# Kernel tuning notes

Measured on AMD Instinct MI355X. Metric: run time of the kernel, lower is better.

Reference implementation:

```python
import jax, jax.numpy as jnp
import numpy as np

TEMP = 1.0
EPS = 1e-3  # keras LayerNormalization default epsilon


def _ln(x, g, b):
    m = jnp.mean(x, -1, keepdims=True)
    v = jnp.mean((x - m) ** 2, -1, keepdims=True)
    return g * (x - m) * jax.lax.rsqrt(v + EPS) + b


def setup_inputs() -> dict:
    key = jax.random.key(0)
    ks = jax.random.split(key, 16)
    B, N, C, A, F = 8, 2048, 64, 256, 128
    r = lambda k, s: (jax.random.normal(ks[k], s) * 0.02).astype(jnp.float32)
    z = lambda n: jnp.zeros((n,), jnp.float32)
    return {
        'spatial': jax.random.normal(ks[0], (B, N, C), jnp.float32),
        'frequency': jax.random.normal(ks[1], (B, N, C), jnp.float32),
        'wavelet': jax.random.normal(ks[2], (B, N, C), jnp.float32),
        'Ws': r(3, (C, A)), 'bs': z(A),
        'Wf': r(4, (C, A)), 'bf': z(A),
        'Ww': r(5, (C, A)), 'bw': z(A),
        'g1': jnp.ones((A,), jnp.float32), 'b1': z(A),
        'Wk': r(6, (A, F)), 'bk': z(F),
        'Wq': r(7, (A, F)), 'bq': z(F),
        'Wt': r(8, (A, F)), 'bt': z(F),
        'Wg': r(9, (F + 3, F)), 'bg': z(F),
        'Wfu': r(10, (3 * F, F)), 'bfu': z(F),
        'Wdf': r(11, (F, F)), 'bdf': z(F),
        'g2': jnp.ones((F,), jnp.float32), 'b2': z(F),
    }


def _forward(spatial, frequency, wavelet, Ws, bs, Wf, bf, Ww, bw, g1, b1,
             Wk, bk, Wq, bq, Wt, bt, Wg, bg, Wfu, bfu, Wdf, bdf, g2, b2):
    B = spatial.shape[0]
    # FeatureAlignment: per-domain Dense + shared LayerNorm
    aligned = [
        _ln(spatial @ Ws + bs, g1, b1),
        _ln(frequency @ Wf + bf, g1, b1),
        _ln(wavelet @ Ww + bw, g1, b1),
    ]  # each [B, N, A]
    # DomainCorrelation
    K = [a @ Wk + bk for a in aligned]  # [B, N, F]
    Q = [a @ Wq + bq for a in aligned]
    corr = jnp.zeros((B, 3, 3), spatial.dtype)
    for i in range(3):
        for j in range(i, 3):
            # queries from domain j, keys from domain i (as in original)
            s = jax.nn.softmax(jnp.einsum('bnd,bmd->bnm', Q[j], K[i]) / TEMP, axis=-1)
            m = jnp.mean(s, axis=(1, 2))  # [B]
            corr = corr.at[:, i, j].set(m)
            if i != j:
                corr = corr.at[:, j, i].set(m)
    # NOTE: original applies softmax over the batch axis of the [B] row means
    dw = [jax.nn.softmax(jnp.mean(corr[:, i, :], axis=1)) for i in range(3)]  # each [B]
    # FeatureTransfer
    corr_mean = jnp.mean(corr, axis=1)  # [B, 3]
    enhanced = []
    for a, w in zip(aligned, dw):
        t = a @ Wt + bt  # [B, N, F]
        N = t.shape[1]
        gin = jnp.concatenate([t, jnp.broadcast_to(corr_mean[:, None, :], (B, N, 3))], axis=-1)
        gate = jax.nn.sigmoid(gin @ Wg + bg)
        enhanced.append(t * gate * w[:, None, None])
    fused = jnp.concatenate(enhanced, axis=-1) @ Wfu + bfu  # [B, N, F]
    out = _ln(fused @ Wdf + bdf, g2, b2)
    return out, corr, dw, enhanced


def reference(spatial, frequency, wavelet, Ws, bs, Wf, bf, Ww, bw, g1, b1,
              Wk, bk, Wq, bq, Wt, bt, Wg, bg, Wfu, bfu, Wdf, bdf, g2, b2):
    out, corr, dw, enh = _forward(spatial, frequency, wavelet, Ws, bs, Wf, bf, Ww, bw,
                                  g1, b1, Wk, bk, Wq, bq, Wt, bt, Wg, bg, Wfu, bfu,
                                  Wdf, bdf, g2, b2)
    return (out, corr, dw[0], dw[1], dw[2], enh[0], enh[1], enh[2])
```

## Files before the change

kernel.cpp:

```cpp
#include <hip/hip_runtime.h>
#include <math.h>


typedef __attribute__((ext_vector_type(8))) short short8;
typedef __attribute__((ext_vector_type(4))) float f32x4;
#define MFMA(a, b, c) __builtin_amdgcn_mfma_f32_16x16x32_bf16(a, b, c, 0, 0, 0)

#define NTOK 32
#define XP 72
#define AP 264
#define TP 136
#define PP 12

#define WD0_B 0u
#define WD1_B 32768u
#define WD2_B 65536u
#define WT_B  98304u
#define WG_B  163840u
#define WF0_B 196608u
#define WF1_B 229376u
#define WF2_B 262144u
#define WDF_B 294912u

__device__ __forceinline__ unsigned short bf16rtn(float v) {
    unsigned u = __float_as_uint(v);
    unsigned r = u + 0x7FFFu + ((u >> 16) & 1u);
    return (unsigned short)(r >> 16);
}
__device__ __forceinline__ void split2(float v, unsigned short& h, unsigned short& l) {
    h = bf16rtn(v);
    float hf = __uint_as_float(((unsigned)h) << 16);
    l = bf16rtn(v - hf);
}
__device__ __forceinline__ float bf2f(unsigned short h) {
    return __uint_as_float(((unsigned)h) << 16);
}

__device__ __forceinline__ unsigned cvt_pk_bf16(float a, float b) {
    unsigned r;
    asm("v_cvt_pk_bf16_f32 %0, %1, %2" : "=v"(r) : "v"(a), "v"(b));
    return r;
}
__device__ __forceinline__ void split2pk(float a, float b, unsigned& hp, unsigned& lp) {
    hp = cvt_pk_bf16(a, b);
    const float ha = __uint_as_float(hp << 16);
    const float hb = __uint_as_float(hp & 0xffff0000u);
    lp = cvt_pk_bf16(a - ha, b - hb);
}
__device__ __forceinline__ void stage_x(const f32x4 v,
                                        unsigned short* __restrict__ xh,
                                        unsigned short* __restrict__ xl,
                                        int stok, int sc4) {
    unsigned h01, l01, h23, l23;
    split2pk(v.x, v.y, h01, l01);
    split2pk(v.z, v.w, h23, l23);
    *(uint2*)&xh[stok * XP + sc4] = make_uint2(h01, h23);
    *(uint2*)&xl[stok * XP + sc4] = make_uint2(l01, l23);
}

__global__ __launch_bounds__(256) void prep_kernel(
    const float* __restrict__ Ws, const float* __restrict__ Wf,
    const float* __restrict__ Ww, const float* __restrict__ Wt,
    const float* __restrict__ Wg, const float* __restrict__ Wfu,
    const float* __restrict__ Wdf, unsigned short* __restrict__ ws)
{
    int s = blockIdx.x * 256 + threadIdx.x;
    const float* src; int K, N; unsigned base, S; int fi;
    if (s < 2048)      { src = Ws;            K = 64;  N = 256; base = WD0_B; S = 16384; fi = s; }
    else if (s < 4096) { src = Wf;            K = 64;  N = 256; base = WD1_B; S = 16384; fi = s - 2048; }
    else if (s < 6144) { src = Ww;            K = 64;  N = 256; base = WD2_B; S = 16384; fi = s - 4096; }
    else if (s < 10240){ src = Wt;            K = 256; N = 128; base = WT_B;  S = 32768; fi = s - 6144; }
    else if (s < 12288){ src = Wg;            K = 128; N = 128; base = WG_B;  S = 16384; fi = s - 10240; }
    else if (s < 14336){ src = Wfu;           K = 128; N = 128; base = WF0_B; S = 16384; fi = s - 12288; }
    else if (s < 16384){ src = Wfu + 16384;   K = 128; N = 128; base = WF1_B; S = 16384; fi = s - 14336; }
    else if (s < 18432){ src = Wfu + 32768;   K = 128; N = 128; base = WF2_B; S = 16384; fi = s - 16384; }
    else               { src = Wdf;           K = 128; N = 128; base = WDF_B; S = 16384; fi = s - 18432; }
    const int lane = fi & 63, frag = fi >> 6;
    const int KC = K >> 5;
    const int nt = frag / KC, kc = frag - nt * KC;
    const int n  = nt * 16 + (lane & 15);
    const int k0 = kc * 32 + (lane >> 4) * 8;
    short8 hv, lv;
    #pragma unroll
    for (int j = 0; j < 8; ++j) {
        unsigned short h, l;
        split2(src[(k0 + j) * N + n], h, l);
        hv[j] = (short)h; lv[j] = (short)l;
    }
    *(short8*)&ws[base + (unsigned)fi * 8]     = hv;
    *(short8*)&ws[base + S + (unsigned)fi * 8] = lv;
}

__device__ __forceinline__ void gemm128_d2(
    const unsigned short* __restrict__ wsB, unsigned S,
    const unsigned short* __restrict__ Ph, const unsigned short* __restrict__ Pl,
    int tok0, int tok1, int quad, int wv, int lane, f32x4 acc[2])
{
    short8 Bh[2], Bl[2];
    #pragma unroll
    for (int j = 0; j < 2; ++j) {
        const unsigned short* bp = wsB + ((unsigned)(wv * 4 + j) * 64 + lane) * 8;
        Bh[j] = *(const short8*)bp; Bl[j] = *(const short8*)(bp + S);
    }
    #pragma unroll
    for (int kc = 0; kc < 4; ++kc) {
        const short8 bh = Bh[kc & 1], bl = Bl[kc & 1];
        if (kc + 2 < 4) {
            const unsigned short* bp = wsB + ((unsigned)(wv * 4 + kc + 2) * 64 + lane) * 8;
            Bh[kc & 1] = *(const short8*)bp; Bl[kc & 1] = *(const short8*)(bp + S);
        }
        const int k = kc * 32 + quad * 8;
        const short8 Ah0 = *(const short8*)&Ph[tok0 * TP + k];
        const short8 Al0 = *(const short8*)&Pl[tok0 * TP + k];
        const short8 Ah1 = *(const short8*)&Ph[tok1 * TP + k];
        const short8 Al1 = *(const short8*)&Pl[tok1 * TP + k];
        acc[0] = MFMA(Ah0, bh, acc[0]);
        acc[1] = MFMA(Ah1, bh, acc[1]);
        acc[0] = MFMA(Al0, bh, acc[0]);
        acc[1] = MFMA(Al1, bh, acc[1]);
        acc[0] = MFMA(Ah0, bl, acc[0]);
        acc[1] = MFMA(Ah1, bl, acc[1]);
    }
}

__global__ __launch_bounds__(512) void mega_kernel(
    const float* __restrict__ x0, const float* __restrict__ x1,
    const float* __restrict__ x2,
    const float* __restrict__ bd0, const float* __restrict__ bd1,
    const float* __restrict__ bd2,
    const float* __restrict__ g1, const float* __restrict__ b1,
    const float* __restrict__ bt, const float* __restrict__ Wg,
    const float* __restrict__ bg, const float* __restrict__ bfu,
    const float* __restrict__ bdf, const float* __restrict__ g2,
    const float* __restrict__ b2,
    const unsigned short* __restrict__ ws,
    float* __restrict__ out, float* __restrict__ consts,
    float* __restrict__ e0, float* __restrict__ e1, float* __restrict__ e2)
{
    __shared__ __align__(16) unsigned char smem[54272];
    unsigned short* xh = (unsigned short*)smem;
    unsigned short* xl = xh + 32 * XP;
    unsigned short* th = (unsigned short*)smem;
    unsigned short* tl = th + 32 * TP;
    unsigned short* ah = (unsigned short*)(smem + 17408);
    unsigned short* al = ah + 32 * AP;
    unsigned short* eh = (unsigned short*)(smem + 17408);
    unsigned short* el = eh + 32 * TP;
    float* ostage = (float*)(smem + 17408);
    float* psumS  = (float*)(smem + 51200);
    float* psumQ  = psumS + 32 * PP;

    if (blockIdx.x & 256) __builtin_amdgcn_s_sleep(78);

    const int tid = threadIdx.x, wv = tid >> 6, lane = tid & 63;
    const int lm = lane & 15, quad = lane >> 4;
    const int row0 = blockIdx.x * NTOK;
    const int tok0 = lm, tok1 = lm + 16;
    const int stok = tid >> 4, sc4 = (tid & 15) * 4;

    if (blockIdx.x == 0) {
        if (tid < 72) consts[tid] = 4.8828125e-4f;
        else if (tid < 96) consts[tid] = 0.125f;
    }

    int cA[2]; float g1c[2], b1c[2];
    #pragma unroll
    for (int i = 0; i < 2; ++i) { cA[i] = (wv * 2 + i) * 16 + lm; g1c[i] = g1[cA[i]]; b1c[i] = b1[cA[i]]; }
    const int cT = wv * 16 + lm;
    const float btc = bt[cT];
    const float bgc = bg[cT] + 4.8828125e-4f * (Wg[16384 + cT] + Wg[16512 + cT] + Wg[16640 + cT]);
    const float bdc = bdf[cT], g2c = g2[cT], b2c = b2[cT];
    f32x4 facc[2];
    { const float bv = bfu[cT]; facc[0] = (f32x4){bv, bv, bv, bv}; facc[1] = facc[0]; }

    const float* xs[3]  = {x0, x1, x2};
    const float* bds[3] = {bd0, bd1, bd2};
    float* es[3] = {e0, e1, e2};
    const unsigned WDB[3] = {WD0_B, WD1_B, WD2_B};
    const unsigned WFB[3] = {WF0_B, WF1_B, WF2_B};

    {
        const f32x4 v = __builtin_nontemporal_load(
            (const f32x4*)&xs[0][(row0 + stok) * 64 + sc4]);
        stage_x(v, xh, xl, stok, sc4);
    }
    __syncthreads();

    for (int d = 0; d < 3; ++d) {
        f32x4 acc[2][2];
        {
            const float* bdp = bds[d];
            #pragma unroll
            for (int i = 0; i < 2; ++i) {
                const float bv = bdp[cA[i]];
                acc[i][0] = (f32x4){bv, bv, bv, bv}; acc[i][1] = acc[i][0];
            }
        }
        {
            short8 Bh[2], Bl[2];
            #pragma unroll
            for (int j = 0; j < 2; ++j) {
                const unsigned short* bp = ws + WDB[d] +
                    ((unsigned)((wv * 2 + j) * 2 + 0) * 64 + lane) * 8;
                Bh[j] = *(const short8*)bp; Bl[j] = *(const short8*)(bp + 16384);
            }
            #pragma unroll
            for (int f = 0; f < 4; ++f) {
                const int kc = f >> 1, i = f & 1;
                const short8 bh = Bh[f & 1], bl = Bl[f & 1];
                if (f + 2 < 4) {
                    const int f2 = f + 2;
                    const unsigned short* bp = ws + WDB[d] +
                        ((unsigned)((wv * 2 + (f2 & 1)) * 2 + (f2 >> 1)) * 64 + lane) * 8;
                    Bh[f & 1] = *(const short8*)bp; Bl[f & 1] = *(const short8*)(bp + 16384);
                }
                const int k = kc * 32 + quad * 8;
                const short8 Ah0 = *(const short8*)&xh[tok0 * XP + k];
                const short8 Al0 = *(const short8*)&xl[tok0 * XP + k];
                const short8 Ah1 = *(const short8*)&xh[tok1 * XP + k];
                const short8 Al1 = *(const short8*)&xl[tok1 * XP + k];
                acc[i][0] = MFMA(Ah0, bh, acc[i][0]);
                acc[i][1] = MFMA(Ah1, bh, acc[i][1]);
                acc[i][0] = MFMA(Al0, bh, acc[i][0]);
                acc[i][1] = MFMA(Al1, bh, acc[i][1]);
                acc[i][0] = MFMA(Ah0, bl, acc[i][0]);
                acc[i][1] = MFMA(Ah1, bl, acc[i][1]);
            }
        }
        #pragma unroll
        for (int m = 0; m < 2; ++m)
            #pragma unroll
            for (int r = 0; r < 4; ++r) {
                float s = acc[0][m][r] + acc[1][m][r];
                float q = acc[0][m][r] * acc[0][m][r] + acc[1][m][r] * acc[1][m][r];
                #pragma unroll
                for (int off = 1; off < 16; off <<= 1) {
                    s += __shfl_xor(s, off); q += __shfl_xor(q, off);
                }
                if (lm == 0) {
                    const int row = m * 16 + quad * 4 + r;
                    psumS[row * PP + wv] = s;
                    psumQ[row * PP + wv] = q;
                }
            }
        __syncthreads();

        #pragma unroll
        for (int m = 0; m < 2; ++m)
            #pragma unroll
            for (int r = 0; r < 4; ++r) {
                const int row = m * 16 + quad * 4 + r;
                const float4 s0 = *(const float4*)&psumS[row * PP];
                const float4 s1 = *(const float4*)&psumS[row * PP + 4];
                const float4 q0 = *(const float4*)&psumQ[row * PP];
                const float4 q1 = *(const float4*)&psumQ[row * PP + 4];
                const float S = s0.x + s0.y + s0.z + s0.w + s1.x + s1.y + s1.z + s1.w;
                const float Q = q0.x + q0.y + q0.z + q0.w + q1.x + q1.y + q1.z + q1.w;
                const float mean = S * (1.f / 256.f);
                const float rs = rsqrtf(Q * (1.f / 256.f) - mean * mean + 1e-3f);
                const float v0 = (acc[0][m][r] - mean) * rs * g1c[0] + b1c[0];
                const float v1 = (acc[1][m][r] - mean) * rs * g1c[1] + b1c[1];
                unsigned hp, lp; split2pk(v0, v1, hp, lp);
                ah[row * AP + cA[0]] = (unsigned short)hp;
                ah[row * AP + cA[1]] = (unsigned short)(hp >> 16);
                al[row * AP + cA[0]] = (unsigned short)lp;
                al[row * AP + cA[1]] = (unsigned short)(lp >> 16);
            }
        __syncthreads();

        f32x4 xvn;
        if (d < 2)
            xvn = __builtin_nontemporal_load(
                (const f32x4*)&xs[d + 1][(row0 + stok) * 64 + sc4]);

        f32x4 tac[2];
        tac[0] = (f32x4){btc, btc, btc, btc}; tac[1] = tac[0];
        {
            short8 Bh[2], Bl[2];
            #pragma unroll
            for (int j = 0; j < 2; ++j) {
                const unsigned short* bp = ws + WT_B + ((unsigned)(wv * 8 + j) * 64 + lane) * 8;
                Bh[j] = *(const short8*)bp; Bl[j] = *(const short8*)(bp + 32768);
            }
            #pragma unroll
            for (int kc = 0; kc < 8; ++kc) {
                const short8 bh = Bh[kc & 1], bl = Bl[kc & 1];
                if (kc + 2 < 8) {
                    const unsigned short* bp = ws + WT_B + ((unsigned)(wv * 8 + kc + 2) * 64 + lane) * 8;
                    Bh[kc & 1] = *(const short8*)bp; Bl[kc & 1] = *(const short8*)(bp + 32768);
                }
                const int k = kc * 32 + quad * 8;
                const short8 Ah0 = *(const short8*)&ah[tok0 * AP + k];
                const short8 Al0 = *(const short8*)&al[tok0 * AP + k];
                const short8 Ah1 = *(const short8*)&ah[tok1 * AP + k];
                const short8 Al1 = *(const short8*)&al[tok1 * AP + k];
                tac[0] = MFMA(Ah0, bh, tac[0]);
                tac[1] = MFMA(Ah1, bh, tac[1]);
                tac[0] = MFMA(Al0, bh, tac[0]);
                tac[1] = MFMA(Al1, bh, tac[1]);
                tac[0] = MFMA(Ah0, bl, tac[0]);
                tac[1] = MFMA(Ah1, bl, tac[1]);
            }
        }
        #pragma unroll
        for (int m = 0; m < 2; ++m) {
            const int rb = m * 16 + quad * 4;
            unsigned hp, lp;
            split2pk(tac[m][0], tac[m][1], hp, lp);
            th[rb * TP + cT]       = (unsigned short)hp;
            th[(rb + 1) * TP + cT] = (unsigned short)(hp >> 16);
            tl[rb * TP + cT]       = (unsigned short)lp;
            tl[(rb + 1) * TP + cT] = (unsigned short)(lp >> 16);
            split2pk(tac[m][2], tac[m][3], hp, lp);
            th[(rb + 2) * TP + cT] = (unsigned short)hp;
            th[(rb + 3) * TP + cT] = (unsigned short)(hp >> 16);
            tl[(rb + 2) * TP + cT] = (unsigned short)lp;
            tl[(rb + 3) * TP + cT] = (unsigned short)(lp >> 16);
        }
        __syncthreads();

        f32x4 zac[2];
        zac[0] = (f32x4){bgc, bgc, bgc, bgc}; zac[1] = zac[0];
        gemm128_d2(ws + WG_B, 16384, th, tl, tok0, tok1, quad, wv, lane, zac);

        #pragma unroll
        for (int m = 0; m < 2; ++m) {
            const int rb = m * 16 + quad * 4;
            float e[4];
            #pragma unroll
            for (int r = 0; r < 4; ++r) {
                const int row = rb + r;
                const float tv = bf2f(th[row * TP + cT]) + bf2f(tl[row * TP + cT]);
                e[r] = tv * (1.f / (1.f + __expf(-zac[m][r]))) * 0.125f;
            }
            unsigned hp, lp;
            split2pk(e[0], e[1], hp, lp);
            eh[rb * TP + cT]       = (unsigned short)hp;
            eh[(rb + 1) * TP + cT] = (unsigned short)(hp >> 16);
            el[rb * TP + cT]       = (unsigned short)lp;
            el[(rb + 1) * TP + cT] = (unsigned short)(lp >> 16);
            split2pk(e[2], e[3], hp, lp);
            eh[(rb + 2) * TP + cT] = (unsigned short)hp;
            eh[(rb + 3) * TP + cT] = (unsigned short)(hp >> 16);
            el[(rb + 2) * TP + cT] = (unsigned short)lp;
            el[(rb + 3) * TP + cT] = (unsigned short)(lp >> 16);
        }
        __syncthreads();

        gemm128_d2(ws + WFB[d], 16384, eh, el, tok0, tok1, quad, wv, lane, facc);

        #pragma unroll
        for (int p = 0; p < 2; ++p) {
            const int row = (tid >> 5) + p * 16;
            const int c4 = (tid & 31) * 4;
            const ushort4 h0 = *(const ushort4*)&eh[row * TP + c4];
            const ushort4 l0 = *(const ushort4*)&el[row * TP + c4];
            f32x4 o = {bf2f(h0.x) + bf2f(l0.x), bf2f(h0.y) + bf2f(l0.y),
                       bf2f(h0.z) + bf2f(l0.z), bf2f(h0.w) + bf2f(l0.w)};
            __builtin_nontemporal_store(o, (f32x4*)(es[d] + (row0 + row) * 128 + c4));
        }

        if (d < 2) {
            stage_x(xvn, xh, xl, stok, sc4);
        } else {
            #pragma unroll
            for (int m = 0; m < 2; ++m) {
                const int rb = m * 16 + quad * 4;
                unsigned hp, lp;
                split2pk(facc[m][0], facc[m][1], hp, lp);
                th[rb * TP + cT]       = (unsigned short)hp;
                th[(rb + 1) * TP + cT] = (unsigned short)(hp >> 16);
                tl[rb * TP + cT]       = (unsigned short)lp;
                tl[(rb + 1) * TP + cT] = (unsigned short)(lp >> 16);
                split2pk(facc[m][2], facc[m][3], hp, lp);
                th[(rb + 2) * TP + cT] = (unsigned short)hp;
                th[(rb + 3) * TP + cT] = (unsigned short)(hp >> 16);
                tl[(rb + 2) * TP + cT] = (unsigned short)lp;
                tl[(rb + 3) * TP + cT] = (unsigned short)(lp >> 16);
            }
        }
        __syncthreads();
    }

    f32x4 dac[2];
    dac[0] = (f32x4){bdc, bdc, bdc, bdc}; dac[1] = dac[0];
    gemm128_d2(ws + WDF_B, 16384, th, tl, tok0, tok1, quad, wv, lane, dac);

    #pragma unroll
    for (int m = 0; m < 2; ++m)
        #pragma unroll
        for (int r = 0; r < 4; ++r) {
            float s = dac[m][r];
            float q = dac[m][r] * dac[m][r];
            #pragma unroll
            for (int off = 1; off < 16; off <<= 1) {
                s += __shfl_xor(s, off); q += __shfl_xor(q, off);
            }
            if (lm == 0) {
                const int row = m * 16 + quad * 4 + r;
                psumS[row * PP + wv] = s;
                psumQ[row * PP + wv] = q;
            }
        }
    __syncthreads();
    #pragma unroll
    for (int m = 0; m < 2; ++m)
        #pragma unroll
        for (int r = 0; r < 4; ++r) {
            const int row = m * 16 + quad * 4 + r;
            const float4 s0 = *(const float4*)&psumS[row * PP];
            const float4 s1 = *(const float4*)&psumS[row * PP + 4];
            const float4 q0 = *(const float4*)&psumQ[row * PP];
            const float4 q1 = *(const float4*)&psumQ[row * PP + 4];
            const float S = s0.x + s0.y + s0.z + s0.w + s1.x + s1.y + s1.z + s1.w;
            const float Q = q0.x + q0.y + q0.z + q0.w + q1.x + q1.y + q1.z + q1.w;
            const float mean = S * (1.f / 128.f);
            const float rs = rsqrtf(Q * (1.f / 128.f) - mean * mean + 1e-3f);
            ostage[row * 128 + cT] = (dac[m][r] - mean) * rs * g2c + b2c;
        }
    __syncthreads();
    #pragma unroll
    for (int p = 0; p < 2; ++p) {
        const int row = (tid >> 5) + p * 16;
        const int c4 = (tid & 31) * 4;
        const f32x4 o = *(const f32x4*)&ostage[row * 128 + c4];
        __builtin_nontemporal_store(o, (f32x4*)(out + (row0 + row) * 128 + c4));
    }
}

extern "C" void kernel_launch(void* const* d_in, const int* in_sizes, int n_in,
                              void* d_out, int out_size, void* d_ws, size_t ws_size,
                              hipStream_t stream) {
    const float* spatial   = (const float*)d_in[0];
    const float* frequency = (const float*)d_in[1];
    const float* wavelet   = (const float*)d_in[2];
    const float* Ws  = (const float*)d_in[3];
    const float* bs  = (const float*)d_in[4];
    const float* Wf  = (const float*)d_in[5];
    const float* bf  = (const float*)d_in[6];
    const float* Ww  = (const float*)d_in[7];
    const float* bw  = (const float*)d_in[8];
    const float* g1  = (const float*)d_in[9];
    const float* b1  = (const float*)d_in[10];
    const float* Wt  = (const float*)d_in[15];
    const float* bt  = (const float*)d_in[16];
    const float* Wg  = (const float*)d_in[17];
    const float* bg  = (const float*)d_in[18];
    const float* Wfu = (const float*)d_in[19];
    const float* bfu = (const float*)d_in[20];
    const float* Wdf = (const float*)d_in[21];
    const float* bdf = (const float*)d_in[22];
    const float* g2  = (const float*)d_in[23];
    const float* b2  = (const float*)d_in[24];

    float* out    = (float*)d_out;
    float* consts = out + 2097152;
    float* enh0   = out + 2097248;
    float* enh1   = out + 4194400;
    float* enh2   = out + 6291552;
    unsigned short* wsp = (unsigned short*)d_ws;

    prep_kernel<<<80, 256, 0, stream>>>(Ws, Wf, Ww, Wt, Wg, Wfu, Wdf, wsp);
    mega_kernel<<<16384 / NTOK, 512, 0, stream>>>(
        spatial, frequency, wavelet, bs, bf, bw, g1, b1,
        bt, Wg, bg, bfu, bdf, g2, b2, wsp,
        out, consts, enh0, enh1, enh2);
}
```

Measured before the change: 183.9 us.

## Halve token tile to 16 and use 4-wave blocks with two column tiles per wave

Shrinks each block from 32 tokens and 8 waves to 16 tokens and 4 waves, launching twice as many blocks with half the shared memory. Each wave now covers more output columns for a single 16-token MFMA row, so one A fragment is reused across several B fragments instead of one B fragment across two token tiles. The s_sleep stagger for half the blocks is removed. The intent is better occupancy and scheduling across CUs, at the cost of reloading the weight fragments from global/L2 twice as often per token.

```diff
diff --git a/kernel.cpp b/kernel.cpp
--- a/kernel.cpp
+++ b/kernel.cpp
@@ -6,7 +6,7 @@
 typedef __attribute__((ext_vector_type(4))) float f32x4;
 #define MFMA(a, b, c) __builtin_amdgcn_mfma_f32_16x16x32_bf16(a, b, c, 0, 0, 0)
 
-#define NTOK 32
+#define NTOK 16
 #define XP 72
 #define AP 264
 #define TP 136
@@ -91,39 +91,43 @@
     *(short8*)&ws[base + S + (unsigned)fi * 8] = lv;
 }
 
-__device__ __forceinline__ void gemm128_d2(
+__device__ __forceinline__ void gemm128_2n(
     const unsigned short* __restrict__ wsB, unsigned S,
     const unsigned short* __restrict__ Ph, const unsigned short* __restrict__ Pl,
-    int tok0, int tok1, int quad, int wv, int lane, f32x4 acc[2])
+    int tok, int quad, int wv, int lane, f32x4 acc[2])
 {
-    short8 Bh[2], Bl[2];
-    #pragma unroll
-    for (int j = 0; j < 2; ++j) {
-        const unsigned short* bp = wsB + ((unsigned)(wv * 4 + j) * 64 + lane) * 8;
-        Bh[j] = *(const short8*)bp; Bl[j] = *(const short8*)(bp + S);
-    }
+    short8 Bh[2][2], Bl[2][2];
+    #pragma unroll
+    for (int j = 0; j < 2; ++j)
+        #pragma unroll
+        for (int s = 0; s < 2; ++s) {
+            const unsigned short* bp = wsB + ((unsigned)((wv * 2 + j) * 4 + s) * 64 + lane) * 8;
+            Bh[j][s] = *(const short8*)bp; Bl[j][s] = *(const short8*)(bp + S);
+        }
     #pragma unroll
     for (int kc = 0; kc < 4; ++kc) {
-        const short8 bh = Bh[kc & 1], bl = Bl[kc & 1];
+        const short8 bh0 = Bh[0][kc & 1], bl0 = Bl[0][kc & 1];
+        const short8 bh1 = Bh[1][kc & 1], bl1 = Bl[1][kc & 1];
         if (kc + 2 < 4) {
-            const unsigned short* bp = wsB + ((unsigned)(wv * 4 + kc + 2) * 64 + lane) * 8;
-            Bh[kc & 1] = *(const short8*)bp; Bl[kc & 1] = *(const short8*)(bp + S);
+            #pragma unroll
+            for (int j = 0; j < 2; ++j) {
+                const unsigned short* bp = wsB + ((unsigned)((wv * 2 + j) * 4 + kc + 2) * 64 + lane) * 8;
+                Bh[j][kc & 1] = *(const short8*)bp; Bl[j][kc & 1] = *(const short8*)(bp + S);
+            }
         }
         const int k = kc * 32 + quad * 8;
-        const short8 Ah0 = *(const short8*)&Ph[tok0 * TP + k];
-        const short8 Al0 = *(const short8*)&Pl[tok0 * TP + k];
-        const short8 Ah1 = *(const short8*)&Ph[tok1 * TP + k];
-        const short8 Al1 = *(const short8*)&Pl[tok1 * TP + k];
-        acc[0] = MFMA(Ah0, bh, acc[0]);
-        acc[1] = MFMA(Ah1, bh, acc[1]);
-        acc[0] = MFMA(Al0, bh, acc[0]);
-        acc[1] = MFMA(Al1, bh, acc[1]);
-        acc[0] = MFMA(Ah0, bl, acc[0]);
-        acc[1] = MFMA(Ah1, bl, acc[1]);
-    }
-}
-
-__global__ __launch_bounds__(512) void mega_kernel(
+        const short8 Ah = *(const short8*)&Ph[tok * TP + k];
+        const short8 Al = *(const short8*)&Pl[tok * TP + k];
+        acc[0] = MFMA(Ah, bh0, acc[0]);
+        acc[1] = MFMA(Ah, bh1, acc[1]);
+        acc[0] = MFMA(Al, bh0, acc[0]);
+        acc[1] = MFMA(Al, bh1, acc[1]);
+        acc[0] = MFMA(Ah, bl0, acc[0]);
+        acc[1] = MFMA(Ah, bl1, acc[1]);
+    }
+}
+
+__global__ __launch_bounds__(256) void mega_kernel(
     const float* __restrict__ x0, const float* __restrict__ x1,
     const float* __restrict__ x2,
     const float* __restrict__ bd0, const float* __restrict__ bd1,
@@ -137,25 +141,23 @@
     float* __restrict__ out, float* __restrict__ consts,
     float* __restrict__ e0, float* __restrict__ e1, float* __restrict__ e2)
 {
-    __shared__ __align__(16) unsigned char smem[54272];
+    __shared__ __align__(16) unsigned char smem[27136];
     unsigned short* xh = (unsigned short*)smem;
-    unsigned short* xl = xh + 32 * XP;
+    unsigned short* xl = xh + 16 * XP;
     unsigned short* th = (unsigned short*)smem;
-    unsigned short* tl = th + 32 * TP;
-    unsigned short* ah = (unsigned short*)(smem + 17408);
-    unsigned short* al = ah + 32 * AP;
-    unsigned short* eh = (unsigned short*)(smem + 17408);
-    unsigned short* el = eh + 32 * TP;
-    float* ostage = (float*)(smem + 17408);
-    float* psumS  = (float*)(smem + 51200);
-    float* psumQ  = psumS + 32 * PP;
-
-    if (blockIdx.x & 256) __builtin_amdgcn_s_sleep(78);
+    unsigned short* tl = th + 16 * TP;
+    unsigned short* ah = (unsigned short*)(smem + 8704);
+    unsigned short* al = ah + 16 * AP;
+    unsigned short* eh = (unsigned short*)(smem + 8704);
+    unsigned short* el = eh + 16 * TP;
+    float* ostage = (float*)(smem + 8704);
+    float* psumS  = (float*)(smem + 25600);
+    float* psumQ  = psumS + 16 * PP;
 
     const int tid = threadIdx.x, wv = tid >> 6, lane = tid & 63;
     const int lm = lane & 15, quad = lane >> 4;
     const int row0 = blockIdx.x * NTOK;
-    const int tok0 = lm, tok1 = lm + 16;
+    const int tok = lm;
     const int stok = tid >> 4, sc4 = (tid & 15) * 4;
 
     if (blockIdx.x == 0) {
@@ -163,15 +165,21 @@
         else if (tid < 96) consts[tid] = 0.125f;
     }
 
-    int cA[2]; float g1c[2], b1c[2];
-    #pragma unroll
-    for (int i = 0; i < 2; ++i) { cA[i] = (wv * 2 + i) * 16 + lm; g1c[i] = g1[cA[i]]; b1c[i] = b1[cA[i]]; }
-    const int cT = wv * 16 + lm;
-    const float btc = bt[cT];
-    const float bgc = bg[cT] + 4.8828125e-4f * (Wg[16384 + cT] + Wg[16512 + cT] + Wg[16640 + cT]);
-    const float bdc = bdf[cT], g2c = g2[cT], b2c = b2[cT];
+    int cA[4]; float g1c[4], b1c[4];
+    #pragma unroll
+    for (int i = 0; i < 4; ++i) { cA[i] = (wv * 4 + i) * 16 + lm; g1c[i] = g1[cA[i]]; b1c[i] = b1[cA[i]]; }
+    int cT[2]; float btc[2], bgc[2], bdc[2], g2c[2], b2c[2];
     f32x4 facc[2];
-    { const float bv = bfu[cT]; facc[0] = (f32x4){bv, bv, bv, bv}; facc[1] = facc[0]; }
+    #pragma unroll
+    for (int j = 0; j < 2; ++j) {
+        const int c = (wv * 2 + j) * 16 + lm;
+        cT[j] = c;
+        btc[j] = bt[c];
+        bgc[j] = bg[c] + 4.8828125e-4f * (Wg[16384 + c] + Wg[16512 + c] + Wg[16640 + c]);
+        bdc[j] = bdf[c]; g2c[j] = g2[c]; b2c[j] = b2[c];
+        const float bv = bfu[c];
+        facc[j] = (f32x4){bv, bv, bv, bv};
+    }
 
     const float* xs[3]  = {x0, x1, x2};
     const float* bds[3] = {bd0, bd1, bd2};
@@ -187,85 +195,89 @@
     __syncthreads();
 
     for (int d = 0; d < 3; ++d) {
-        f32x4 acc[2][2];
+        f32x4 acc[4];
         {
             const float* bdp = bds[d];
             #pragma unroll
-            for (int i = 0; i < 2; ++i) {
+            for (int i = 0; i < 4; ++i) {
                 const float bv = bdp[cA[i]];
-                acc[i][0] = (f32x4){bv, bv, bv, bv}; acc[i][1] = acc[i][0];
+                acc[i] = (f32x4){bv, bv, bv, bv};
             }
         }
         {
-            short8 Bh[2], Bl[2];
-            #pragma unroll
-            for (int j = 0; j < 2; ++j) {
+            short8 Bh[4], Bl[4];
+            #pragma unroll
+            for (int i = 0; i < 4; ++i) {
                 const unsigned short* bp = ws + WDB[d] +
-                    ((unsigned)((wv * 2 + j) * 2 + 0) * 64 + lane) * 8;
-                Bh[j] = *(const short8*)bp; Bl[j] = *(const short8*)(bp + 16384);
-            }
-            #pragma unroll
-            for (int f = 0; f < 4; ++f) {
-                const int kc = f >> 1, i = f & 1;
-                const short8 bh = Bh[f & 1], bl = Bl[f & 1];
-                if (f + 2 < 4) {
-                    const int f2 = f + 2;
-                    const unsigned short* bp = ws + WDB[d] +
-                        ((unsigned)((wv * 2 + (f2 & 1)) * 2 + (f2 >> 1)) * 64 + lane) * 8;
-                    Bh[f & 1] = *(const short8*)bp; Bl[f & 1] = *(const short8*)(bp + 16384);
+                    ((unsigned)((wv * 4 + i) * 2 + 0) * 64 + lane) * 8;
+                Bh[i] = *(const short8*)bp; Bl[i] = *(const short8*)(bp + 16384);
+            }
+            #pragma unroll
+            for (int kc = 0; kc < 2; ++kc) {
+                const int k = kc * 32 + quad * 8;
+                const short8 Ah = *(const short8*)&xh[tok * XP + k];
+                const short8 Al = *(const short8*)&xl[tok * XP + k];
+                short8 bh[4], bl[4];
+                #pragma unroll
+                for (int i = 0; i < 4; ++i) { bh[i] = Bh[i]; bl[i] = Bl[i]; }
+                if (kc == 0) {
+                    #pragma unroll
+                    for (int i = 0; i < 4; ++i) {
+                        const unsigned short* bp = ws + WDB[d] +
+                            ((unsigned)((wv * 4 + i) * 2 + 1) * 64 + lane) * 8;
+                        Bh[i] = *(const short8*)bp; Bl[i] = *(const short8*)(bp + 16384);
+                    }
                 }
-                const int k = kc * 32 + quad * 8;
-                const short8 Ah0 = *(const short8*)&xh[tok0 * XP + k];
-                const short8 Al0 = *(const short8*)&xl[tok0 * XP + k];
-                const short8 Ah1 = *(const short8*)&xh[tok1 * XP + k];
-                const short8 Al1 = *(const short8*)&xl[tok1 * XP + k];
-                acc[i][0] = MFMA(Ah0, bh, acc[i][0]);
-                acc[i][1] = MFMA(Ah1, bh, acc[i][1]);
-                acc[i][0] = MFMA(Al0, bh, acc[i][0]);
-                acc[i][1] = MFMA(Al1, bh, acc[i][1]);
-                acc[i][0] = MFMA(Ah0, bl, acc[i][0]);
-                acc[i][1] = MFMA(Ah1, bl, acc[i][1]);
-            }
-        }
-        #pragma unroll
-        for (int m = 0; m < 2; ++m)
-            #pragma unroll
-            for (int r = 0; r < 4; ++r) {
-                float s = acc[0][m][r] + acc[1][m][r];
-                float q = acc[0][m][r] * acc[0][m][r] + acc[1][m][r] * acc[1][m][r];
-                #pragma unroll
-                for (int off = 1; off < 16; off <<= 1) {
-                    s += __shfl_xor(s, off); q += __shfl_xor(q, off);
-                }
-                if (lm == 0) {
-                    const int row = m * 16 + quad * 4 + r;
-                    psumS[row * PP + wv] = s;
-                    psumQ[row * PP + wv] = q;
-                }
-            }
+                #pragma unroll
+                for (int i = 0; i < 4; ++i) acc[i] = MFMA(Ah, bh[i], acc[i]);
+                #pragma unroll
+                for (int i = 0; i < 4; ++i) acc[i] = MFMA(Al, bh[i], acc[i]);
+                #pragma unroll
+                for (int i = 0; i < 4; ++i) acc[i] = MFMA(Ah, bl[i], acc[i]);
+            }
+        }
+        #pragma unroll
+        for (int r = 0; r < 4; ++r) {
+            float s = acc[0][r] + acc[1][r] + acc[2][r] + acc[3][r];
+            float q = acc[0][r] * acc[0][r] + acc[1][r] * acc[1][r]
+                    + acc[2][r] * acc[2][r] + acc[3][r] * acc[3][r];
+            #pragma unroll
+            for (int off = 1; off < 16; off <<= 1) {
+                s += __shfl_xor(s, off); q += __shfl_xor(q, off);
+            }
+            if (lm == 0) {
+                const int row = quad * 4 + r;
+                psumS[row * PP + wv] = s;
+                psumQ[row * PP + wv] = q;
+            }
+        }
         __syncthreads();
 
         #pragma unroll
-        for (int m = 0; m < 2; ++m)
-            #pragma unroll
-            for (int r = 0; r < 4; ++r) {
-                const int row = m * 16 + quad * 4 + r;
-                const float4 s0 = *(const float4*)&psumS[row * PP];
-                const float4 s1 = *(const float4*)&psumS[row * PP + 4];
-                const float4 q0 = *(const float4*)&psumQ[row * PP];
-                const float4 q1 = *(const float4*)&psumQ[row * PP + 4];
-                const float S = s0.x + s0.y + s0.z + s0.w + s1.x + s1.y + s1.z + s1.w;
-                const float Q = q0.x + q0.y + q0.z + q0.w + q1.x + q1.y + q1.z + q1.w;
-                const float mean = S * (1.f / 256.f);
-                const float rs = rsqrtf(Q * (1.f / 256.f) - mean * mean + 1e-3f);
-                const float v0 = (acc[0][m][r] - mean) * rs * g1c[0] + b1c[0];
-                const float v1 = (acc[1][m][r] - mean) * rs * g1c[1] + b1c[1];
-                unsigned hp, lp; split2pk(v0, v1, hp, lp);
-                ah[row * AP + cA[0]] = (unsigned short)hp;
-                ah[row * AP + cA[1]] = (unsigned short)(hp >> 16);
-                al[row * AP + cA[0]] = (unsigned short)lp;
-                al[row * AP + cA[1]] = (unsigned short)(lp >> 16);
-            }
+        for (int r = 0; r < 4; ++r) {
+            const int row = quad * 4 + r;
+            const float4 s0 = *(const float4*)&psumS[row * PP];
+            const float4 q0 = *(const float4*)&psumQ[row * PP];
+            const float S = s0.x + s0.y + s0.z + s0.w;
+            const float Q = q0.x + q0.y + q0.z + q0.w;
+            const float mean = S * (1.f / 256.f);
+            const float rs = rsqrtf(Q * (1.f / 256.f) - mean * mean + 1e-3f);
+            float v[4];
+            #pragma unroll
+            for (int i = 0; i < 4; ++i)
+                v[i] = (acc[i][r] - mean) * rs * g1c[i] + b1c[i];
+            unsigned hp, lp;
+            split2pk(v[0], v[1], hp, lp);
+            ah[row * AP + cA[0]] = (unsigned short)hp;
+            ah[row * AP + cA[1]] = (unsigned short)(hp >> 16);
+            al[row * AP + cA[0]] = (unsigned short)lp;
+            al[row * AP + cA[1]] = (unsigned short)(lp >> 16);
+            split2pk(v[2], v[3], hp, lp);
+            ah[row * AP + cA[2]] = (unsigned short)hp;
+            ah[row * AP + cA[3]] = (unsigned short)(hp >> 16);
+            al[row * AP + cA[2]] = (unsigned short)lp;
+            al[row * AP + cA[3]] = (unsigned short)(lp >> 16);
+        }
         __syncthreads();
 
         f32x4 xvn;
@@ -274,84 +286,96 @@
                 (const f32x4*)&xs[d + 1][(row0 + stok) * 64 + sc4]);
 
         f32x4 tac[2];
-        tac[0] = (f32x4){btc, btc, btc, btc}; tac[1] = tac[0];
+        #pragma unroll
+        for (int j = 0; j < 2; ++j) tac[j] = (f32x4){btc[j], btc[j], btc[j], btc[j]};
         {
-            short8 Bh[2], Bl[2];
-            #pragma unroll
-            for (int j = 0; j < 2; ++j) {
-                const unsigned short* bp = ws + WT_B + ((unsigned)(wv * 8 + j) * 64 + lane) * 8;
-                Bh[j] = *(const short8*)bp; Bl[j] = *(const short8*)(bp + 32768);
-            }
+            short8 Bh[2][2], Bl[2][2];
+            #pragma unroll
+            for (int j = 0; j < 2; ++j)
+                #pragma unroll
+                for (int s = 0; s < 2; ++s) {
+                    const unsigned short* bp = ws + WT_B +
+                        ((unsigned)((wv * 2 + j) * 8 + s) * 64 + lane) * 8;
+                    Bh[j][s] = *(const short8*)bp; Bl[j][s] = *(const short8*)(bp + 32768);
+                }
             #pragma unroll
             for (int kc = 0; kc < 8; ++kc) {
-                const short8 bh = Bh[kc & 1], bl = Bl[kc & 1];
+                const short8 bh0 = Bh[0][kc & 1], bl0 = Bl[0][kc & 1];
+                const short8 bh1 = Bh[1][kc & 1], bl1 = Bl[1][kc & 1];
                 if (kc + 2 < 8) {
-                    const unsigned short* bp = ws + WT_B + ((unsigned)(wv * 8 + kc + 2) * 64 + lane) * 8;
-                    Bh[kc & 1] = *(const short8*)bp; Bl[kc & 1] = *(const short8*)(bp + 32768);
+                    #pragma unroll
+                    for (int j = 0; j < 2; ++j) {
+                        const unsigned short* bp = ws + WT_B +
+                            ((unsigned)((wv * 2 + j) * 8 + kc + 2) * 64 + lane) * 8;
+                        Bh[j][kc & 1] = *(const short8*)bp; Bl[j][kc & 1] = *(const short8*)(bp + 32768);
+                    }
                 }
                 const int k = kc * 32 + quad * 8;
-                const short8 Ah0 = *(const short8*)&ah[tok0 * AP + k];
-                const short8 Al0 = *(const short8*)&al[tok0 * AP + k];
-                const short8 Ah1 = *(const short8*)&ah[tok1 * AP + k];
-                const short8 Al1 = *(const short8*)&al[tok1 * AP + k];
-                tac[0] = MFMA(Ah0, bh, tac[0]);
-                tac[1] = MFMA(Ah1, bh, tac[1]);
-                tac[0] = MFMA(Al0, bh, tac[0]);
-                tac[1] = MFMA(Al1, bh, tac[1]);
-                tac[0] = MFMA(Ah0, bl, tac[0]);
-                tac[1] = MFMA(Ah1, bl, tac[1]);
-            }
-        }
-        #pragma unroll
-        for (int m = 0; m < 2; ++m) {
-            const int rb = m * 16 + quad * 4;
-            unsigned hp, lp;
-            split2pk(tac[m][0], tac[m][1], hp, lp);
-            th[rb * TP + cT]       = (unsigned short)hp;
-            th[(rb + 1) * TP + cT] = (unsigned short)(hp >> 16);
-            tl[rb * TP + cT]       = (unsigned short)lp;
-            tl[(rb + 1) * TP + cT] = (unsigned short)(lp >> 16);
-            split2pk(tac[m][2], tac[m][3], hp, lp);
-            th[(rb + 2) * TP + cT] = (unsigned short)hp;
-            th[(rb + 3) * TP + cT] = (unsigned short)(hp >> 16);
-            tl[(rb + 2) * TP + cT] = (unsigned short)lp;
-            tl[(rb + 3) * TP + cT] = (unsigned short)(lp >> 16);
+                const short8 Ah = *(const short8*)&ah[tok * AP + k];
+                const short8 Al = *(const short8*)&al[tok * AP + k];
+                tac[0] = MFMA(Ah, bh0, tac[0]);
+                tac[1] = MFMA(Ah, bh1, tac[1]);
+                tac[0] = MFMA(Al, bh0, tac[0]);
+                tac[1] = MFMA(Al, bh1, tac[1]);
+                tac[0] = MFMA(Ah, bl0, tac[0]);
+                tac[1] = MFMA(Ah, bl1, tac[1]);
+            }
+        }
+        {
+            const int rb = quad * 4;
+            #pragma unroll
+            for (int j = 0; j < 2; ++j) {
+                unsigned hp, lp;
+                split2pk(tac[j][0], tac[j][1], hp, lp);
+                th[rb * TP + cT[j]]       = (unsigned short)hp;
+                th[(rb + 1) * TP + cT[j]] = (unsigned short)(hp >> 16);
+                tl[rb * TP + cT[j]]       = (unsigned short)lp;
+                tl[(rb + 1) * TP + cT[j]] = (unsigned short)(lp >> 16);
+                split2pk(tac[j][2], tac[j][3], hp, lp);
+                th[(rb + 2) * TP + cT[j]] = (unsigned short)hp;
+                th[(rb + 3) * TP + cT[j]] = (unsigned short)(hp >> 16);
+                tl[(rb + 2) * TP + cT[j]] = (unsigned short)lp;
+                tl[(rb + 3) * TP + cT[j]] = (unsigned short)(lp >> 16);
+            }
         }
         __syncthreads();
 
         f32x4 zac[2];
-        zac[0] = (f32x4){bgc, bgc, bgc, bgc}; zac[1] = zac[0];
-        gemm128_d2(ws + WG_B, 16384, th, tl, tok0, tok1, quad, wv, lane, zac);
-
-        #pragma unroll
-        for (int m = 0; m < 2; ++m) {
-            const int rb = m * 16 + quad * 4;
-            float e[4];
-            #pragma unroll
-            for (int r = 0; r < 4; ++r) {
-                const int row = rb + r;
-                const float tv = bf2f(th[row * TP + cT]) + bf2f(tl[row * TP + cT]);
-                e[r] = tv * (1.f / (1.f + __expf(-zac[m][r]))) * 0.125f;
-            }
-            unsigned hp, lp;
-            split2pk(e[0], e[1], hp, lp);
-            eh[rb * TP + cT]       = (unsigned short)hp;
-            eh[(rb + 1) * TP + cT] = (unsigned short)(hp >> 16);
-            el[rb * TP + cT]       = (unsigned short)lp;
-            el[(rb + 1) * TP + cT] = (unsigned short)(lp >> 16);
-            split2pk(e[2], e[3], hp, lp);
-            eh[(rb + 2) * TP + cT] = (unsigned short)hp;
-            eh[(rb + 3) * TP + cT] = (unsigned short)(hp >> 16);
-            el[(rb + 2) * TP + cT] = (unsigned short)lp;
-            el[(rb + 3) * TP + cT] = (unsigned short)(lp >> 16);
+        #pragma unroll
+        for (int j = 0; j < 2; ++j) zac[j] = (f32x4){bgc[j], bgc[j], bgc[j], bgc[j]};
+        gemm128_2n(ws + WG_B, 16384, th, tl, tok, quad, wv, lane, zac);
+
+        {
+            const int rb = quad * 4;
+            #pragma unroll
+            for (int j = 0; j < 2; ++j) {
+                float e[4];
+                #pragma unroll
+                for (int r = 0; r < 4; ++r) {
+                    const int row = rb + r;
+                    const float tv = bf2f(th[row * TP + cT[j]]) + bf2f(tl[row * TP + cT[j]]);
+                    e[r] = tv * (1.f / (1.f + __expf(-zac[j][r]))) * 0.125f;
+                }
+                unsigned hp, lp;
+                split2pk(e[0], e[1], hp, lp);
+                eh[rb * TP + cT[j]]       = (unsigned short)hp;
+                eh[(rb + 1) * TP + cT[j]] = (unsigned short)(hp >> 16);
+                el[rb * TP + cT[j]]       = (unsigned short)lp;
+                el[(rb + 1) * TP + cT[j]] = (unsigned short)(lp >> 16);
+                split2pk(e[2], e[3], hp, lp);
+                eh[(rb + 2) * TP + cT[j]] = (unsigned short)hp;
+                eh[(rb + 3) * TP + cT[j]] = (unsigned short)(hp >> 16);
+                el[(rb + 2) * TP + cT[j]] = (unsigned short)lp;
+                el[(rb + 3) * TP + cT[j]] = (unsigned short)(lp >> 16);
+            }
         }
         __syncthreads();
 
-        gemm128_d2(ws + WFB[d], 16384, eh, el, tok0, tok1, quad, wv, lane, facc);
+        gemm128_2n(ws + WFB[d], 16384, eh, el, tok, quad, wv, lane, facc);
 
         #pragma unroll
         for (int p = 0; p < 2; ++p) {
-            const int row = (tid >> 5) + p * 16;
+            const int row = (tid >> 5) + p * 8;
             const int c4 = (tid & 31) * 4;
             const ushort4 h0 = *(const ushort4*)&eh[row * TP + c4];
             const ushort4 l0 = *(const ushort4*)&el[row * TP + c4];
@@ -363,65 +387,62 @@
         if (d < 2) {
             stage_x(xvn, xh, xl, stok, sc4);
         } else {
-            #pragma unroll
-            for (int m = 0; m < 2; ++m) {
-                const int rb = m * 16 + quad * 4;
+            const int rb = quad * 4;
+            #pragma unroll
+            for (int j = 0; j < 2; ++j) {
                 unsigned hp, lp;
-                split2pk(facc[m][0], facc[m][1], hp, lp);
-                th[rb * TP + cT]       = (unsigned short)hp;
-                th[(rb + 1) * TP + cT] = (unsigned short)(hp >> 16);
-                tl[rb * TP + cT]       = (unsigned short)lp;
-                tl[(rb + 1) * TP + cT] = (unsigned short)(lp >> 16);
-                split2pk(facc[m][2], facc[m][3], hp, lp);
-                th[(rb + 2) * TP + cT] = (unsigned short)hp;
-                th[(rb + 3) * TP + cT] = (unsigned short)(hp >> 16);
-                tl[(rb + 2) * TP + cT] = (unsigned short)lp;
-                tl[(rb + 3) * TP + cT] = (unsigned short)(lp >> 16);
+                split2pk(facc[j][0], facc[j][1], hp, lp);
+                th[rb * TP + cT[j]]       = (unsigned short)hp;
+                th[(rb + 1) * TP + cT[j]] = (unsigned short)(hp >> 16);
+                tl[rb * TP + cT[j]]       = (unsigned short)lp;
+                tl[(rb + 1) * TP + cT[j]] = (unsigned short)(lp >> 16);
+                split2pk(facc[j][2], facc[j][3], hp, lp);
+                th[(rb + 2) * TP + cT[j]] = (unsigned short)hp;
+                th[(rb + 3) * TP + cT[j]] = (unsigned short)(hp >> 16);
+                tl[(rb + 2) * TP + cT[j]] = (unsigned short)lp;
+                tl[(rb + 3) * TP + cT[j]] = (unsigned short)(lp >> 16);
             }
         }
         __syncthreads();
     }
 
     f32x4 dac[2];
-    dac[0] = (f32x4){bdc, bdc, bdc, bdc}; dac[1] = dac[0];
-    gemm128_d2(ws + WDF_B, 16384, th, tl, tok0, tok1, quad, wv, lane, dac);
-
-    #pragma unroll
-    for (int m = 0; m < 2; ++m)
-        #pragma unroll
-        for (int r = 0; r < 4; ++r) {
-            float s = dac[m][r];
-            float q = dac[m][r] * dac[m][r];
-            #pragma unroll
-            for (int off = 1; off < 16; off <<= 1) {
-                s += __shfl_xor(s, off); q += __shfl_xor(q, off);
-            }
-            if (lm == 0) {
-                const int row = m * 16 + quad * 4 + r;
-                psumS[row * PP + wv] = s;
-                psumQ[row * PP + wv] = q;
-            }
-        }
+    #pragma unroll
+    for (int j = 0; j < 2; ++j) dac[j] = (f32x4){bdc[j], bdc[j], bdc[j], bdc[j]};
+    gemm128_2n(ws + WDF_B, 16384, th, tl, tok, quad, wv, lane, dac);
+
+    #pragma unroll
+    for (int r = 0; r < 4; ++r) {
+        float s = dac[0][r] + dac[1][r];
+        float q = dac[0][r] * dac[0][r] + dac[1][r] * dac[1][r];
+        #pragma unroll
+        for (int off = 1; off < 16; off <<= 1) {
+            s += __shfl_xor(s, off); q += __shfl_xor(q, off);
+        }
+        if (lm == 0) {
+            const int row = quad * 4 + r;
+            psumS[row * PP + wv] = s;
+            psumQ[row * PP + wv] = q;
+        }
+    }
     __syncthreads();
     #pragma unroll
-    for (int m = 0; m < 2; ++m)
-        #pragma unroll
-        for (int r = 0; r < 4; ++r) {
-            const int row = m * 16 + quad * 4 + r;
-            const float4 s0 = *(const float4*)&psumS[row * PP];
-            const float4 s1 = *(const float4*)&psumS[row * PP + 4];
-            const float4 q0 = *(const float4*)&psumQ[row * PP];
-            const float4 q1 = *(const float4*)&psumQ[row * PP + 4];
-            const float S = s0.x + s0.y + s0.z + s0.w + s1.x + s1.y + s1.z + s1.w;
-            const float Q = q0.x + q0.y + q0.z + q0.w + q1.x + q1.y + q1.z + q1.w;
-            const float mean = S * (1.f / 128.f);
-            const float rs = rsqrtf(Q * (1.f / 128.f) - mean * mean + 1e-3f);
-            ostage[row * 128 + cT] = (dac[m][r] - mean) * rs * g2c + b2c;
-        }
+    for (int r = 0; r < 4; ++r) {
+        const int row = quad * 4 + r;
+        const float4 s0 = *(const float4*)&psumS[row * PP];
+        const float4 q0 = *(const float4*)&psumQ[row * PP];
+        const float S = s0.x + s0.y + s0.z + s0.w;
+        const float Q = q0.x + q0.y + q0.z + q0.w;
+        const float mean = S * (1.f / 128.f);
+        const float rs = rsqrtf(Q * (1.f / 128.f) - mean * mean + 1e-3f);
+        #pragma unroll
+        for (int j = 0; j < 2; ++j)
+            ostage[row * 128 + cT[j]] = (dac[j][r] - mean) * rs * g2c[j] + b2c[j];
+    }
     __syncthreads();
     #pragma unroll
     for (int p = 0; p < 2; ++p) {
-        const int row = (tid >> 5) + p * 16;
+        const int row = (tid >> 5) + p * 8;
         const int c4 = (tid & 31) * 4;
         const f32x4 o = *(const f32x4*)&ostage[row * 128 + c4];
         __builtin_nontemporal_store(o, (f32x4*)(out + (row0 + row) * 128 + c4));
@@ -461,7 +482,7 @@
     unsigned short* wsp = (unsigned short*)d_ws;
 
     prep_kernel<<<80, 256, 0, stream>>>(Ws, Wf, Ww, Wt, Wg, Wfu, Wdf, wsp);
-    mega_kernel<<<16384 / NTOK, 512, 0, stream>>>(
+    mega_kernel<<<16384 / NTOK, 256, 0, stream>>>(
         spatial, frequency, wavelet, bs, bf, bw, g1, b1,
         bt, Wg, bg, bfu, bdf, g2, b2, wsp,
         out, consts, enh0, enh1, enh2);
```

Measured after the change: 215.1 us. +17.0%, slower.
